# Optimization experiments

Hardware: AMD Instinct MI355X
Metric: run time of the kernel (lower is better)

Reference implementation:

```python
import jax, jax.numpy as jnp
import numpy as np

FEAT = 320        # in_channel == out_channel, LayerNorm dim
NPTS = 2048       # num_points == Conv1d channels (proj_dim)
TEMP = FEAT ** 0.5
EPS = 1e-5


def setup_inputs() -> dict:
    key = jax.random.key(0)
    ks = jax.random.split(key, 7)
    B = 32
    query = jax.random.normal(ks[0], (B, FEAT, NPTS), dtype=jnp.float32)
    support = jax.random.normal(ks[1], (B, FEAT, NPTS), dtype=jnp.float32)
    # Conv1d(2048, 2048, 1, bias=False) weights, squeezed to [out, in]
    s = 1.0 / np.sqrt(NPTS)
    Wq = jax.random.uniform(ks[2], (NPTS, NPTS), jnp.float32, -s, s)
    Wk = jax.random.uniform(ks[3], (NPTS, NPTS), jnp.float32, -s, s)
    Wv = jax.random.uniform(ks[4], (NPTS, NPTS), jnp.float32, -s, s)
    gamma = jnp.ones((FEAT,), jnp.float32)
    beta = jnp.zeros((FEAT,), jnp.float32)
    return {"query": query, "support": support, "Wq": Wq, "Wk": Wk,
            "Wv": Wv, "gamma": gamma, "beta": beta}


def reference(query, support, Wq, Wk, Wv, gamma, beta):
    # query, support: [B, FEAT=320, NPTS=2048]
    # 1x1 Conv1d on x.transpose(1,2) -> q[b,o,l] = sum_i W[o,i] * x[b,l,i]
    q = jnp.einsum('oi,bfi->bof', Wq, support)   # [B, NPTS, FEAT]
    k = jnp.einsum('oi,bfi->bof', Wk, query)     # [B, NPTS, FEAT]
    v = jnp.einsum('oi,bfi->bof', Wv, query)     # [B, NPTS, FEAT]
    # attn[b,l,m] = sum_o q[b,o,l] * k[b,o,m] / sqrt(FEAT)
    attn = jnp.einsum('bol,bom->blm', q, k) / TEMP   # [B, FEAT, FEAT]
    attn = jax.nn.softmax(attn, axis=-1)
    # query_output[b,l,o] = sum_m attn[b,l,m] * v[b,o,m]
    query_output = jnp.einsum('blm,bom->blo', attn, v)  # [B, FEAT, NPTS]
    # residual + LayerNorm over the FEAT (=320) axis
    up = (query_output + query).transpose(0, 2, 1)      # [B, NPTS, FEAT]
    mu = jnp.mean(up, axis=-1, keepdims=True)
    var = jnp.var(up, axis=-1, keepdims=True)
    normed = (up - mu) * jax.lax.rsqrt(var + EPS) * gamma + beta
    return normed.transpose(0, 2, 1)                    # [B, FEAT, NPTS]
```

## Files before the change

kernel.cpp:

```cpp
#include <hip/hip_runtime.h>

typedef _Float16 f16;
typedef _Float16 f16x4 __attribute__((ext_vector_type(4)));
typedef _Float16 f16x8 __attribute__((ext_vector_type(8)));
typedef float    f32x4 __attribute__((ext_vector_type(4)));

#define NB    32
#define FEAT  320
#define NPTS  2048
#define M1    (NB * FEAT)
#define KDIM  2048

__device__ __forceinline__ void stage16(f16* lds_base, const f16* g) {
    __builtin_amdgcn_global_load_lds(
        (const __attribute__((address_space(1))) void*)g,
        (__attribute__((address_space(3))) void*)lds_base, 16, 0, 0);
}

__global__ void cast_k(const float* __restrict__ src, f16* __restrict__ dst, int n4) {
    int i = blockIdx.x * blockDim.x + threadIdx.x;
    int stride = gridDim.x * blockDim.x;
    for (; i < n4; i += stride) {
        f32x4 v = *(const f32x4*)(src + (size_t)i * 4);
        *(f16x4*)(dst + (size_t)i * 4) = __builtin_convertvector(v, f16x4);
    }
}

__global__ void castT_k(const float* __restrict__ Wq, const float* __restrict__ Wk,
                        f16* __restrict__ WqT, f16* __restrict__ WkT) {
    __shared__ float T[64][65];
    const float* W = blockIdx.z ? Wk : Wq;
    f16* WT        = blockIdx.z ? WkT : WqT;
    const int i0 = blockIdx.x * 64, o0 = blockIdx.y * 64;
    const int tid = threadIdx.x;
#pragma unroll
    for (int j = 0; j < 4; ++j) {
        int e = j * 256 + tid, r = e >> 4, c4 = e & 15;
        f32x4 v = *(const f32x4*)&W[(size_t)(o0 + r) * 2048 + i0 + c4 * 4];
        *(f32x4*)&T[r][c4 * 4] = v;
    }
    __syncthreads();
#pragma unroll
    for (int j = 0; j < 2; ++j) {
        int e = j * 256 + tid, ir = e >> 3, oc8 = e & 7;
        f16x8 val;
#pragma unroll
        for (int k = 0; k < 8; ++k) val[k] = (f16)T[oc8 * 8 + k][ir];
        *(f16x8*)&WT[(size_t)(i0 + ir) * 2048 + o0 + oc8 * 8] = val;
    }
}

__global__ void cast_q_dual(const float* __restrict__ q, f16* __restrict__ qf16,
                            f16* __restrict__ qT16) {
    __shared__ float T[64][65];
    const int b = blockIdx.z;
    const int j0 = blockIdx.x * 64, m0 = blockIdx.y * 64;
    const int tid = threadIdx.x;
#pragma unroll
    for (int j = 0; j < 4; ++j) {
        int e = j * 256 + tid, r = e >> 4, c4 = e & 15;
        size_t src = ((size_t)b * FEAT + m0 + r) * NPTS + j0 + c4 * 4;
        f32x4 v = *(const f32x4*)&q[src];
        *(f32x4*)&T[r][c4 * 4] = v;
        *(f16x4*)&qf16[src] = __builtin_convertvector(v, f16x4);
    }
    __syncthreads();
#pragma unroll
    for (int j = 0; j < 2; ++j) {
        int e = j * 256 + tid, jr = e >> 3, mc8 = e & 7;
        f16x8 val;
#pragma unroll
        for (int k = 0; k < 8; ++k) val[k] = (f16)T[mc8 * 8 + k][jr];
        *(f16x8*)&qT16[((size_t)b * NPTS + j0 + jr) * FEAT + m0 + mc8 * 8] = val;
    }
}

__global__ __launch_bounds__(256, 2) void gemm128_f16(
    const f16* __restrict__ A, const f16* __restrict__ B, f16* __restrict__ C,
    float scale) {
    __shared__ f16 As[2 * 128 * 32];
    __shared__ f16 Bs[2 * 128 * 32];
    const int tid = threadIdx.x, lane = tid & 63, w = tid >> 6;
    const int wm = w >> 1, wn = w & 1, lo = lane & 15, q4 = lane >> 4;
    const long tm = (long)blockIdx.y * 128, tn = (long)blockIdx.x * 128;
    const f16* Abase = A + tm * KDIM;
    const f16* Bbase = B + tn * KDIM;
    f32x4 acc[4][4] = {};
    const int srow = lane >> 2, sch = (lane & 3) * 8;

    for (int k0 = 0; k0 < KDIM; k0 += 64) {
#pragma unroll
        for (int j = 0; j < 4; ++j) {
            const int u = w * 4 + j, h = u & 1, Rb = u >> 1;
            const int base = h * 4096 + Rb * 512;
            const long grow = Rb * 16 + srow;
            const long gk = k0 + h * 32 + sch;
            stage16(&As[base], Abase + grow * KDIM + gk);
            stage16(&Bs[base], Bbase + grow * KDIM + gk);
        }
        __syncthreads();
        f16x8 af[4][2], bf[4][2];
#pragma unroll
        for (int s = 0; s < 2; ++s) {
#pragma unroll
            for (int mi = 0; mi < 4; ++mi)
                af[mi][s] = *(const f16x8*)&As[s * 4096 + (wm * 64 + mi * 16 + lo) * 32 + q4 * 8];
#pragma unroll
            for (int ni = 0; ni < 4; ++ni)
                bf[ni][s] = *(const f16x8*)&Bs[s * 4096 + (wn * 64 + ni * 16 + lo) * 32 + q4 * 8];
        }
#pragma unroll
        for (int s = 0; s < 2; ++s)
#pragma unroll
            for (int mi = 0; mi < 4; ++mi)
#pragma unroll
                for (int ni = 0; ni < 4; ++ni)
                    acc[mi][ni] = __builtin_amdgcn_mfma_f32_16x16x32_f16(af[mi][s], bf[ni][s], acc[mi][ni], 0, 0, 0);
        __syncthreads();
    }
#pragma unroll
    for (int mi = 0; mi < 4; ++mi)
#pragma unroll
        for (int ni = 0; ni < 4; ++ni) {
            long gc = tn + wn * 64 + ni * 16 + lo;
#pragma unroll
            for (int r = 0; r < 4; ++r) {
                long gr = tm + wm * 64 + mi * 16 + q4 * 4 + r;
                C[gr * KDIM + gc] = (f16)(acc[mi][ni][r] * scale);
            }
        }
}

__global__ __launch_bounds__(256, 2) void gemm128_res(
    const f16* __restrict__ A, const f16* __restrict__ B,
    const float* __restrict__ query, float* __restrict__ out) {
    __shared__ f16 As[2 * 128 * 32];
    __shared__ f16 Bs[2 * 128 * 32];
    const int tid = threadIdx.x, lane = tid & 63, w = tid >> 6;
    const int wm = w >> 1, wn = w & 1, lo = lane & 15, q4 = lane >> 4;
    const long tm = (long)blockIdx.y * 128, tn = (long)blockIdx.x * 128;
    const f16* Abase = A + tm * KDIM;
    const f16* Bbase = B + tn * KDIM;
    f32x4 acc[4][4] = {};
    const int srow = lane >> 2, sch = (lane & 3) * 8;

    for (int k0 = 0; k0 < KDIM; k0 += 64) {
#pragma unroll
        for (int j = 0; j < 4; ++j) {
            const int u = w * 4 + j, h = u & 1, Rb = u >> 1;
            const int base = h * 4096 + Rb * 512;
            const long grow = Rb * 16 + srow;
            const long gk = k0 + h * 32 + sch;
            stage16(&As[base], Abase + grow * KDIM + gk);
            stage16(&Bs[base], Bbase + grow * KDIM + gk);
        }
        __syncthreads();
        f16x8 af[4][2], bf[4][2];
#pragma unroll
        for (int s = 0; s < 2; ++s) {
#pragma unroll
            for (int mi = 0; mi < 4; ++mi)
                af[mi][s] = *(const f16x8*)&As[s * 4096 + (wm * 64 + mi * 16 + lo) * 32 + q4 * 8];
#pragma unroll
            for (int ni = 0; ni < 4; ++ni)
                bf[ni][s] = *(const f16x8*)&Bs[s * 4096 + (wn * 64 + ni * 16 + lo) * 32 + q4 * 8];
        }
#pragma unroll
        for (int s = 0; s < 2; ++s)
#pragma unroll
            for (int mi = 0; mi < 4; ++mi)
#pragma unroll
                for (int ni = 0; ni < 4; ++ni)
                    acc[mi][ni] = __builtin_amdgcn_mfma_f32_16x16x32_f16(af[mi][s], bf[ni][s], acc[mi][ni], 0, 0, 0);
        __syncthreads();
    }
#pragma unroll
    for (int mi = 0; mi < 4; ++mi)
#pragma unroll
        for (int ni = 0; ni < 4; ++ni) {
            long gc = tn + wn * 64 + ni * 16 + lo;
#pragma unroll
            for (int r = 0; r < 4; ++r) {
                long gr = tm + wm * 64 + mi * 16 + q4 * 4 + r;
                size_t idx = (size_t)gr * KDIM + gc;
                out[idx] = acc[mi][ni][r] + query[idx];
            }
        }
}

__global__ __launch_bounds__(256, 2) void attn_gemm(
    const f16* __restrict__ T, const f16* __restrict__ qf16, float* __restrict__ attn) {
    __shared__ f16 As[2 * 64 * 32];
    __shared__ f16 Bs[2 * 64 * 32];
    const int b = blockIdx.z;
    const long tl = (long)blockIdx.y * 64, tmm = (long)blockIdx.x * 64;
    const int tid = threadIdx.x, lane = tid & 63, w = tid >> 6;
    const int wm = w >> 1, wn = w & 1, lo = lane & 15, q4 = lane >> 4;
    const f16* Abase = T + ((long)b * FEAT + tl) * KDIM;
    const f16* Bbase = qf16 + ((long)b * FEAT + tmm) * KDIM;
    const int srow = lane >> 2, sch = (lane & 3) * 8;
    f32x4 acc[2][2] = {};
    for (int k0 = 0; k0 < KDIM; k0 += 64) {
#pragma unroll
        for (int j = 0; j < 2; ++j) {
            const int u = w * 2 + j, h = u & 1, Rb = u >> 1;
            const int base = h * 2048 + Rb * 512;
            const long grow = Rb * 16 + srow;
            const long gk = k0 + h * 32 + sch;
            stage16(&As[base], Abase + grow * KDIM + gk);
            stage16(&Bs[base], Bbase + grow * KDIM + gk);
        }
        __syncthreads();
        f16x8 af[2][2], bf[2][2];
#pragma unroll
        for (int s = 0; s < 2; ++s) {
#pragma unroll
            for (int mi = 0; mi < 2; ++mi)
                af[mi][s] = *(const f16x8*)&As[s * 2048 + (wm * 32 + mi * 16 + lo) * 32 + q4 * 8];
#pragma unroll
            for (int ni = 0; ni < 2; ++ni)
                bf[ni][s] = *(const f16x8*)&Bs[s * 2048 + (wn * 32 + ni * 16 + lo) * 32 + q4 * 8];
        }
#pragma unroll
        for (int s = 0; s < 2; ++s)
#pragma unroll
            for (int mi = 0; mi < 2; ++mi)
#pragma unroll
                for (int ni = 0; ni < 2; ++ni)
                    acc[mi][ni] = __builtin_amdgcn_mfma_f32_16x16x32_f16(af[mi][s], bf[ni][s], acc[mi][ni], 0, 0, 0);
        __syncthreads();
    }
#pragma unroll
    for (int mi = 0; mi < 2; ++mi)
#pragma unroll
        for (int ni = 0; ni < 2; ++ni) {
            long gm = tmm + wn * 32 + ni * 16 + lo;
#pragma unroll
            for (int r = 0; r < 4; ++r) {
                long gl = tl + wm * 32 + mi * 16 + q4 * 4 + r;
                attn[(long)b * (FEAT * FEAT) + gl * FEAT + gm] = acc[mi][ni][r];
            }
        }
}

__global__ __launch_bounds__(256, 2) void u_gemm(
    const f16* __restrict__ P, const f16* __restrict__ qT16, f16* __restrict__ U) {
    __shared__ f16 As[2 * 64 * 32];
    __shared__ f16 Bs[2 * 128 * 32];
    const int b = blockIdx.z;
    const long tl = (long)blockIdx.y * 64, to = (long)blockIdx.x * 128;
    const int tid = threadIdx.x, lane = tid & 63, w = tid >> 6;
    const int wm = w >> 1, wn = w & 1, lo = lane & 15, q4 = lane >> 4;
    const f16* Abase = P + ((long)b * FEAT + tl) * FEAT;
    const f16* Bbase = qT16 + ((long)b * NPTS + to) * FEAT;
    const int srow = lane >> 2, sch = (lane & 3) * 8;
    f32x4 acc[2][4] = {};
    for (int k0 = 0; k0 < FEAT; k0 += 64) {
#pragma unroll
        for (int j = 0; j < 2; ++j) {
            const int u = w * 2 + j, h = u & 1, Rb = u >> 1;
            stage16(&As[h * 2048 + Rb * 512],
                    Abase + (long)(Rb * 16 + srow) * FEAT + k0 + h * 32 + sch);
        }
#pragma unroll
        for (int j = 0; j < 4; ++j) {
            const int u = w * 4 + j, h = u & 1, Rb = u >> 1;
            stage16(&Bs[h * 4096 + Rb * 512],
                    Bbase + (long)(Rb * 16 + srow) * FEAT + k0 + h * 32 + sch);
        }
        __syncthreads();
        f16x8 af[2][2], bf[4][2];
#pragma unroll
        for (int s = 0; s < 2; ++s) {
#pragma unroll
            for (int mi = 0; mi < 2; ++mi)
                af[mi][s] = *(const f16x8*)&As[s * 2048 + (wm * 32 + mi * 16 + lo) * 32 + q4 * 8];
#pragma unroll
            for (int ni = 0; ni < 4; ++ni)
                bf[ni][s] = *(const f16x8*)&Bs[s * 4096 + (wn * 64 + ni * 16 + lo) * 32 + q4 * 8];
        }
#pragma unroll
        for (int s = 0; s < 2; ++s)
#pragma unroll
            for (int mi = 0; mi < 2; ++mi)
#pragma unroll
                for (int ni = 0; ni < 4; ++ni)
                    acc[mi][ni] = __builtin_amdgcn_mfma_f32_16x16x32_f16(af[mi][s], bf[ni][s], acc[mi][ni], 0, 0, 0);
        __syncthreads();
    }
#pragma unroll
    for (int mi = 0; mi < 2; ++mi)
#pragma unroll
        for (int ni = 0; ni < 4; ++ni) {
            long go = to + wn * 64 + ni * 16 + lo;
#pragma unroll
            for (int r = 0; r < 4; ++r) {
                long gl = tl + wm * 32 + mi * 16 + q4 * 4 + r;
                U[((long)b * FEAT + gl) * NPTS + go] = (f16)acc[mi][ni][r];
            }
        }
}

__global__ void softmax_k(const float* __restrict__ attn, f16* __restrict__ probs) {
    const int r = blockIdx.x * 4 + (threadIdx.x >> 6);
    const int lane = threadIdx.x & 63;
    const float* row = attn + (size_t)r * FEAT;
    float v[5];
    float mx = -1e30f;
#pragma unroll
    for (int j = 0; j < 5; ++j) { v[j] = row[lane + j * 64]; mx = fmaxf(mx, v[j]); }
#pragma unroll
    for (int off = 32; off; off >>= 1) mx = fmaxf(mx, __shfl_xor(mx, off, 64));
    float s = 0.f;
#pragma unroll
    for (int j = 0; j < 5; ++j) { v[j] = __expf(v[j] - mx); s += v[j]; }
#pragma unroll
    for (int off = 32; off; off >>= 1) s += __shfl_xor(s, off, 64);
    const float inv = 1.f / s;
    f16* prow = probs + (size_t)r * FEAT;
#pragma unroll
    for (int j = 0; j < 5; ++j) prow[lane + j * 64] = (f16)(v[j] * inv);
}

__global__ void ln_k(float* __restrict__ out, const float* __restrict__ gamma,
                     const float* __restrict__ beta) {
    __shared__ float g[FEAT], bt[FEAT];
    const int tid = threadIdx.x;
    for (int i = tid; i < FEAT; i += 256) { g[i] = gamma[i]; bt[i] = beta[i]; }
    __syncthreads();
    const int col = blockIdx.x * 256 + tid;
    const int b = col >> 11, o = col & 2047;
    float* base = out + (size_t)b * (FEAT * NPTS) + o;
    float s = 0.f, ss = 0.f;
    for (int l = 0; l < FEAT; ++l) {
        float x = base[(size_t)l * NPTS];
        s += x; ss += x * x;
    }
    const float mu = s * (1.f / FEAT);
    const float var = ss * (1.f / FEAT) - mu * mu;
    const float rstd = rsqrtf(var + 1e-5f);
    for (int l = 0; l < FEAT; ++l) {
        float x = base[(size_t)l * NPTS];
        base[(size_t)l * NPTS] = (x - mu) * rstd * g[l] + bt[l];
    }
}

extern "C" void kernel_launch(void* const* d_in, const int* in_sizes, int n_in,
                              void* d_out, int out_size, void* d_ws, size_t ws_size,
                              hipStream_t stream) {
    const float* query   = (const float*)d_in[0];
    const float* support = (const float*)d_in[1];
    const float* Wq      = (const float*)d_in[2];
    const float* Wk      = (const float*)d_in[3];
    const float* Wv      = (const float*)d_in[4];
    const float* gamma   = (const float*)d_in[5];
    const float* beta    = (const float*)d_in[6];
    float* out = (float*)d_out;

    char* ws = (char*)d_ws;
    const size_t SZ_W = (size_t)KDIM * KDIM * sizeof(f16);
    const size_t SZ_X = (size_t)M1 * KDIM * sizeof(f16);
    f16* wqT  = (f16*)(ws);
    f16* wkT  = (f16*)(ws + SZ_W);
    f16* wv16 = (f16*)(ws + 2 * SZ_W);
    f16* gt   = (f16*)(ws + 3 * SZ_W);
    f16* sf16 = (f16*)(ws + 4 * SZ_W);
    f16* qf16 = (f16*)(ws + 4 * SZ_W + SZ_X);
    f16* qT16 = (f16*)(ws + 4 * SZ_W + 2 * SZ_X);
    f16* T    = (f16*)(ws + 4 * SZ_W + 3 * SZ_X);
    float* attn = (float*)(ws);
    f16*   P    = qf16;
    f16*   U    = sf16;

    const float inv_temp = 0.05590169943749474f;

    castT_k<<<dim3(32, 32, 2), 256, 0, stream>>>(Wq, Wk, wqT, wkT);
    cast_k<<<1024, 256, 0, stream>>>(Wv, wv16, (KDIM * KDIM) / 4);
    cast_k<<<2048, 256, 0, stream>>>(support, sf16, (M1 * KDIM) / 4);
    cast_q_dual<<<dim3(32, 5, 32), 256, 0, stream>>>(query, qf16, qT16);

    gemm128_f16<<<dim3(16, 16), 256, 0, stream>>>(wkT, wqT, gt, inv_temp);
    gemm128_f16<<<dim3(16, 80), 256, 0, stream>>>(sf16, gt, T, 1.0f);
    attn_gemm<<<dim3(5, 5, 32), 256, 0, stream>>>(T, qf16, attn);
    softmax_k<<<2560, 256, 0, stream>>>(attn, P);
    u_gemm<<<dim3(16, 5, 32), 256, 0, stream>>>(P, qT16, U);
    gemm128_res<<<dim3(16, 80), 256, 0, stream>>>(U, wv16, query, out);
    ln_k<<<256, 256, 0, stream>>>(out, gamma, beta);
}
```

Before: 694.9 us.

## Replace 128x128 GEMMs with 320x256 double-buffered swizzled 512-thread GEMM

The two large M=10240 GEMMs (sf16·gt and U·Wv with residual) move to a templated kernel with 320x256 tiles, 8 waves, and double-buffered LDS whose prefetch of the next K slab is interleaved with MFMA phases. It also adds an XOR swizzle on LDS rows to avoid bank conflicts and raises wave priority with s_setprio during MFMA bursts. The larger tile cuts global reloads per FLOP but uses about 144KB of LDS and many accumulator registers, which may limit occupancy. The grid also drops to 256 blocks, which is close to the CU count.

```diff
diff --git a/kernel.cpp b/kernel.cpp
--- a/kernel.cpp
+++ b/kernel.cpp
@@ -131,59 +131,128 @@
         }
 }
 
-__global__ __launch_bounds__(256, 2) void gemm128_res(
+template<int RES>
+__global__ __launch_bounds__(512, 2) void gemm_big(
     const f16* __restrict__ A, const f16* __restrict__ B,
-    const float* __restrict__ query, float* __restrict__ out) {
-    __shared__ f16 As[2 * 128 * 32];
-    __shared__ f16 Bs[2 * 128 * 32];
+    const float* __restrict__ resid, void* __restrict__ outp) {
+    __shared__ f16 As[2][320 * 64];
+    __shared__ f16 Bs[2][256 * 64];
     const int tid = threadIdx.x, lane = tid & 63, w = tid >> 6;
-    const int wm = w >> 1, wn = w & 1, lo = lane & 15, q4 = lane >> 4;
-    const long tm = (long)blockIdx.y * 128, tn = (long)blockIdx.x * 128;
-    const f16* Abase = A + tm * KDIM;
-    const f16* Bbase = B + tn * KDIM;
-    f32x4 acc[4][4] = {};
-    const int srow = lane >> 2, sch = (lane & 3) * 8;
-
-    for (int k0 = 0; k0 < KDIM; k0 += 64) {
-#pragma unroll
-        for (int j = 0; j < 4; ++j) {
-            const int u = w * 4 + j, h = u & 1, Rb = u >> 1;
-            const int base = h * 4096 + Rb * 512;
-            const long grow = Rb * 16 + srow;
-            const long gk = k0 + h * 32 + sch;
-            stage16(&As[base], Abase + grow * KDIM + gk);
-            stage16(&Bs[base], Bbase + grow * KDIM + gk);
-        }
-        __syncthreads();
-        f16x8 af[4][2], bf[4][2];
-#pragma unroll
-        for (int s = 0; s < 2; ++s) {
-#pragma unroll
-            for (int mi = 0; mi < 4; ++mi)
-                af[mi][s] = *(const f16x8*)&As[s * 4096 + (wm * 64 + mi * 16 + lo) * 32 + q4 * 8];
-#pragma unroll
-            for (int ni = 0; ni < 4; ++ni)
-                bf[ni][s] = *(const f16x8*)&Bs[s * 4096 + (wn * 64 + ni * 16 + lo) * 32 + q4 * 8];
-        }
-#pragma unroll
-        for (int s = 0; s < 2; ++s)
-#pragma unroll
-            for (int mi = 0; mi < 4; ++mi)
-#pragma unroll
-                for (int ni = 0; ni < 4; ++ni)
-                    acc[mi][ni] = __builtin_amdgcn_mfma_f32_16x16x32_f16(af[mi][s], bf[ni][s], acc[mi][ni], 0, 0, 0);
-        __syncthreads();
-    }
-#pragma unroll
-    for (int mi = 0; mi < 4; ++mi)
+    const int wm = w >> 2, wn = w & 3, lo = lane & 15, q4 = lane >> 4;
+    const int key = lo & 7;
+    const long bm0 = (long)blockIdx.y * 320, bn0 = (long)blockIdx.x * 256;
+    const int r8 = lane >> 3, sw = (lane & 7) ^ r8;
+    const f16* srcA = A + (bm0 + r8) * KDIM + sw * 8;
+    const f16* srcB = B + (bn0 + r8) * KDIM + sw * 8;
+    const int rA = (wm * 160 + lo) * 64;
+    const int rB = (wn * 64 + lo) * 64;
+    const int sl0 = (q4 ^ key) * 8;
+    const int sl1 = ((q4 | 4) ^ key) * 8;
+
+    f32x4 acc[10][4] = {};
+
+#pragma unroll
+    for (int i = 0; i < 5; ++i)
+        stage16(&As[0][(w + 8 * i) * 512], srcA + (long)(w + 8 * i) * (8 * KDIM));
+#pragma unroll
+    for (int i = 0; i < 4; ++i)
+        stage16(&Bs[0][(w + 8 * i) * 512], srcB + (long)(w + 8 * i) * (8 * KDIM));
+    asm volatile("s_waitcnt vmcnt(0)" ::: "memory");
+    __builtin_amdgcn_s_barrier();
+    asm volatile("" ::: "memory");
+
+    for (int t = 0; t < KDIM / 64; ++t) {
+        const int cur = t & 1, nb = cur ^ 1;
+        const long k0n = (long)(t + 1) * 64;
+        const bool pf = (t + 1 < KDIM / 64);
+        const f16* a = As[cur];
+        const f16* b = Bs[cur];
+        f16x8 af[5], bf[4];
+#pragma unroll
+        for (int ni = 0; ni < 4; ++ni) bf[ni] = *(const f16x8*)&b[rB + ni * 1024 + sl0];
+#pragma unroll
+        for (int i = 0; i < 5; ++i) af[i] = *(const f16x8*)&a[rA + i * 1024 + sl0];
+        if (pf) {
+#pragma unroll
+            for (int i = 0; i < 3; ++i)
+                stage16(&As[nb][(w + 8 * i) * 512], srcA + (long)(w + 8 * i) * (8 * KDIM) + k0n);
+        }
+        __builtin_amdgcn_s_barrier();
+        __builtin_amdgcn_s_setprio(1);
+#pragma unroll
+        for (int i = 0; i < 5; ++i)
+#pragma unroll
+            for (int ni = 0; ni < 4; ++ni)
+                acc[i][ni] = __builtin_amdgcn_mfma_f32_16x16x32_f16(af[i], bf[ni], acc[i][ni], 0, 0, 0);
+        __builtin_amdgcn_s_setprio(0);
+        __builtin_amdgcn_s_barrier();
+#pragma unroll
+        for (int i = 0; i < 5; ++i) af[i] = *(const f16x8*)&a[rA + (5 + i) * 1024 + sl0];
+        if (pf) {
+#pragma unroll
+            for (int i = 3; i < 5; ++i)
+                stage16(&As[nb][(w + 8 * i) * 512], srcA + (long)(w + 8 * i) * (8 * KDIM) + k0n);
+        }
+        __builtin_amdgcn_s_barrier();
+        __builtin_amdgcn_s_setprio(1);
+#pragma unroll
+        for (int i = 0; i < 5; ++i)
+#pragma unroll
+            for (int ni = 0; ni < 4; ++ni)
+                acc[5 + i][ni] = __builtin_amdgcn_mfma_f32_16x16x32_f16(af[i], bf[ni], acc[5 + i][ni], 0, 0, 0);
+        __builtin_amdgcn_s_setprio(0);
+        __builtin_amdgcn_s_barrier();
+#pragma unroll
+        for (int ni = 0; ni < 4; ++ni) bf[ni] = *(const f16x8*)&b[rB + ni * 1024 + sl1];
+#pragma unroll
+        for (int i = 0; i < 5; ++i) af[i] = *(const f16x8*)&a[rA + i * 1024 + sl1];
+        if (pf) {
+#pragma unroll
+            for (int i = 0; i < 4; ++i)
+                stage16(&Bs[nb][(w + 8 * i) * 512], srcB + (long)(w + 8 * i) * (8 * KDIM) + k0n);
+        }
+        __builtin_amdgcn_s_barrier();
+        __builtin_amdgcn_s_setprio(1);
+#pragma unroll
+        for (int i = 0; i < 5; ++i)
+#pragma unroll
+            for (int ni = 0; ni < 4; ++ni)
+                acc[i][ni] = __builtin_amdgcn_mfma_f32_16x16x32_f16(af[i], bf[ni], acc[i][ni], 0, 0, 0);
+        __builtin_amdgcn_s_setprio(0);
+        __builtin_amdgcn_s_barrier();
+#pragma unroll
+        for (int i = 0; i < 5; ++i) af[i] = *(const f16x8*)&a[rA + (5 + i) * 1024 + sl1];
+        __builtin_amdgcn_s_barrier();
+        __builtin_amdgcn_s_setprio(1);
+#pragma unroll
+        for (int i = 0; i < 5; ++i)
+#pragma unroll
+            for (int ni = 0; ni < 4; ++ni)
+                acc[5 + i][ni] = __builtin_amdgcn_mfma_f32_16x16x32_f16(af[i], bf[ni], acc[5 + i][ni], 0, 0, 0);
+        __builtin_amdgcn_s_setprio(0);
+        asm volatile("s_waitcnt vmcnt(0)" ::: "memory");
+        __builtin_amdgcn_s_barrier();
+        asm volatile("" ::: "memory");
+    }
+
+#pragma unroll
+    for (int mi = 0; mi < 10; ++mi)
 #pragma unroll
         for (int ni = 0; ni < 4; ++ni) {
-            long gc = tn + wn * 64 + ni * 16 + lo;
-#pragma unroll
-            for (int r = 0; r < 4; ++r) {
-                long gr = tm + wm * 64 + mi * 16 + q4 * 4 + r;
-                size_t idx = (size_t)gr * KDIM + gc;
-                out[idx] = acc[mi][ni][r] + query[idx];
+            const long gc = bn0 + wn * 64 + ni * 16 + lo;
+            const long gr0 = bm0 + wm * 160 + mi * 16 + q4 * 4;
+            if (RES) {
+                float* out = (float*)outp;
+#pragma unroll
+                for (int r = 0; r < 4; ++r) {
+                    size_t idx = (size_t)(gr0 + r) * KDIM + gc;
+                    out[idx] = acc[mi][ni][r] + resid[idx];
+                }
+            } else {
+                f16* out = (f16*)outp;
+#pragma unroll
+                for (int r = 0; r < 4; ++r)
+                    out[(size_t)(gr0 + r) * KDIM + gc] = (f16)acc[mi][ni][r];
             }
         }
 }
@@ -380,10 +449,10 @@
     cast_q_dual<<<dim3(32, 5, 32), 256, 0, stream>>>(query, qf16, qT16);
 
     gemm128_f16<<<dim3(16, 16), 256, 0, stream>>>(wkT, wqT, gt, inv_temp);
-    gemm128_f16<<<dim3(16, 80), 256, 0, stream>>>(sf16, gt, T, 1.0f);
+    gemm_big<0><<<dim3(8, 32), 512, 0, stream>>>(sf16, gt, nullptr, T);
     attn_gemm<<<dim3(5, 5, 32), 256, 0, stream>>>(T, qf16, attn);
     softmax_k<<<2560, 256, 0, stream>>>(attn, P);
     u_gemm<<<dim3(16, 5, 32), 256, 0, stream>>>(P, qT16, U);
-    gemm128_res<<<dim3(16, 80), 256, 0, stream>>>(U, wv16, query, out);
+    gemm_big<1><<<dim3(8, 32), 512, 0, stream>>>(U, wv16, query, out);
     ln_k<<<256, 256, 0, stream>>>(out, gamma, beta);
 }
```

After: 681.5 us. Within noise of the previous version (-1.9%).
